# Optimization experiments

Hardware: AMD Instinct MI355X
Metric: run time of the kernel (lower is better)

The kernel has to match this reference:

```python
import jax, jax.numpy as jnp
import numpy as np

RHO = 1060.0   # blood density kg/m^3
DX = 1e-3      # grid spacing
CCFL = 0.9     # CFL number
EPS_A = 1e-6   # area floor


def setup_inputs() -> dict:
    key = jax.random.key(0)
    k0, k1, k2 = jax.random.split(key, 3)
    M = 90000          # 3 vessels x 30000 cells
    T = 150            # time steps
    Rs = jax.random.normal(k0, (4,), dtype=jnp.float32)
    sim_dat = jnp.ones((2, M), dtype=jnp.float32)            # row0: A, row1: Q seed
    sim_dat_const = jax.random.uniform(k1, (11, M), dtype=jnp.float32)
    input_data = jax.random.uniform(k2, (T,), dtype=jnp.float32)
    strides = jnp.array([[0, 30000], [30000, 60000], [60000, 90000]], dtype=jnp.int32)
    return {"Rs": Rs, "sim_dat": sim_dat, "sim_dat_const": sim_dat_const,
            "input_data": input_data, "strides": strides, "upper": T}


def reference(Rs, sim_dat, sim_dat_const, input_data, strides, upper):
    M = sim_dat.shape[1]
    # --- SimDense: softplus reparam of 4 resistance scale factors ---
    rs = jax.nn.softplus(Rs)
    idx = jnp.arange(M)
    m1 = (idx >= strides[1, 0]) & (idx < strides[1, 1])  # vessel 1 region
    m2 = (idx >= strides[2, 0]) & (idx < strides[2, 1])  # vessel 2 region
    # constant rows (shifted positive)
    A0 = sim_dat_const[0] + 0.5     # reference area
    beta = sim_dat_const[1] + 1.0   # wall stiffness
    R1 = sim_dat_const[7] + 0.5     # proximal resistance (VAR_INDEX_1)
    R2 = sim_dat_const[8] + 0.5     # distal resistance (VAR_INDEX_2)
    # scatter scaled resistances into vessel-1 / vessel-2 regions
    R1 = jnp.where(m1, rs[0] * R1, jnp.where(m2, rs[2] * R1, R1))
    R2 = jnp.where(m1, rs[1] * R2, jnp.where(m2, rs[3] * R2, R2))
    Rtot = R1 + R2

    A_init = sim_dat[0]
    Q_init = 0.1 * sim_dat[1]
    starts = strides[:, 0]
    ends = strides[:, 1] - 1
    mids = (strides[:, 0] + strides[:, 1]) // 2

    def step(carry, inflow):
        A, Q = carry
        A = jnp.maximum(A, EPS_A)
        sq = jnp.sqrt(A / A0)
        P = beta * (sq - 1.0)                 # tube-law pressure
        u = Q / A
        c = jnp.sqrt(0.5 * beta / RHO * sq)   # wave speed
        smax = jnp.max(jnp.abs(u) + c)
        dt = CCFL * DX / smax                 # CFL-limited timestep
        # conservative fluxes for (A, Q)
        F_A = Q
        F_Q = Q * u + beta / (3.0 * RHO * A0) * A * sq
        # Lax-Friedrichs interface fluxes
        fhA = 0.5 * (F_A[:-1] + F_A[1:]) - 0.5 * smax * (A[1:] - A[:-1])
        fhQ = 0.5 * (F_Q[:-1] + F_Q[1:]) - 0.5 * smax * (Q[1:] - Q[:-1])
        lam = dt / DX
        A_new = A.at[1:-1].add(-lam * (fhA[1:] - fhA[:-1]))
        Q_new = Q.at[1:-1].add(-lam * (fhQ[1:] - fhQ[:-1]))
        # inlet / junction BC: prescribed inflow at each vessel start
        Q_new = Q_new.at[starts].set(inflow)
        # outlet BC: resistive Windkessel Q = P / (R1 + R2)
        Q_new = Q_new.at[ends].set(P[ends] / Rtot[ends])
        A_new = jnp.maximum(A_new, EPS_A)
        return (A_new, Q_new), P[mids]          # record mid-vessel pressures

    _, p = jax.lax.scan(step, (A_init, Q_init), input_data)
    return p  # [upper, 3]
```

## Files before the change

kernel.cpp:

```cpp
#include <hip/hip_runtime.h>

static constexpr int MM  = 90000;
static constexpr int TT  = 150;
static constexpr int BS  = 256;
static constexpr int CPT = 4;
static constexpr int CPB = BS * CPT;
static constexpr int NB  = (MM + CPB - 1) / CPB;
static constexpr int WPB = BS / 64;
static constexpr int PAGE_U32 = 2048;
static constexpr int PAGE_U64 = 1024;

__device__ unsigned int       g_bmax_s[128][PAGE_U32];
__device__ unsigned long long g_edge_s[NB][PAGE_U64];
__device__ unsigned long long g_dummy64;

__device__ __forceinline__ float softplus_f(float x) {
    return fmaxf(x, 0.0f) + log1pf(expf(-fabsf(x)));
}
__device__ __forceinline__ unsigned long long packAQ(float A, float Q) {
    return ((unsigned long long)__float_as_uint(Q) << 32) | (unsigned long long)__float_as_uint(A);
}
#define AG_LOAD32(p)     __hip_atomic_load((p), __ATOMIC_RELAXED, __HIP_MEMORY_SCOPE_AGENT)
#define AG_LOAD64(p)     __hip_atomic_load((p), __ATOMIC_RELAXED, __HIP_MEMORY_SCOPE_AGENT)
#define AG_STORE32(p, v) __hip_atomic_store((p), (v), __ATOMIC_RELAXED, __HIP_MEMORY_SCOPE_AGENT)
#define AG_STORE64(p, v) __hip_atomic_store((p), (v), __ATOMIC_RELAXED, __HIP_MEMORY_SCOPE_AGENT)

__global__ void init_ws_kernel() {
    int i = blockIdx.x * blockDim.x + threadIdx.x;
    int stride = gridDim.x * blockDim.x;
    unsigned int* pb = &g_bmax_s[0][0];
    for (int j = i; j < 128 * PAGE_U32; j += stride)
        pb[j] = ((j / PAGE_U32) < NB) ? 0u : 1u;
    unsigned long long* pe = &g_edge_s[0][0];
    for (int j = i; j < NB * PAGE_U64; j += stride) pe[j] = 0ull;
    if (i == 0) g_dummy64 = ~0ull;
}

__global__ void __launch_bounds__(BS) sim_kernel(
    const float* __restrict__ Rs,
    const float* __restrict__ sim_dat,
    const float* __restrict__ sdc,
    const float* __restrict__ inflow,
    float* __restrict__ out)
{
    __shared__ float sE[2][WPB][2][3];
    __shared__ float sred[2][WPB];
    __shared__ float s_smaxv;
    __shared__ float s_hL[3], s_hR[3];
    __shared__ float s_inflow[TT];

    const int b    = blockIdx.x;
    const int tid  = threadIdx.x;
    const int wv   = tid >> 6;
    const int lane = tid & 63;
    const int base = b * CPB + tid * CPT;

    for (int j = tid; j < TT; j += BS) s_inflow[j] = inflow[j];

    float A[CPT], Q[CPT], A0v[CPT], bet[CPT], cbv[CPT], k2v[CPT], sq[CPT], FQ[CPT];
    bool  act[CPT];
    #pragma unroll
    for (int c = 0; c < CPT; ++c) {
        int i = base + c;
        act[c] = (i < MM);
        if (act[c]) {
            A[c]   = fmaxf(sim_dat[i], 1e-6f);
            Q[c]   = 0.1f * sim_dat[MM + i];
            A0v[c] = sdc[i] + 0.5f;
            bet[c] = sdc[MM + i] + 1.0f;
        } else { A[c] = 1.0f; Q[c] = 0.0f; A0v[c] = 1.0f; bet[c] = 1.0f; }
        cbv[c] = (0.5f * bet[c]) / 1060.0f;
        k2v[c] = bet[c] / (3180.0f * A0v[c]);
    }
    const bool isStart = (base == 0) | (base == 30000) | (base == 60000);
    const bool isEnd   = (base + 3 == 29999) | (base + 3 == 59999) | (base + 3 == 89999);
    const int midSlot = (base == 15000) ? 0 : (base == 45000) ? 1 : (base == 75000) ? 2 : -1;
    float Rtot = 1.0f;
    if (isEnd) {
        int i3 = base + 3;
        float R1 = sdc[7 * MM + i3] + 0.5f;
        float R2 = sdc[8 * MM + i3] + 0.5f;
        if (i3 == 59999)      { R1 *= softplus_f(Rs[0]); R2 *= softplus_f(Rs[1]); }
        else if (i3 == 89999) { R1 *= softplus_f(Rs[2]); R2 *= softplus_f(Rs[3]); }
        Rtot = R1 + R2;
    }

    const bool pubL = (tid == 0) && (b > 0);
    const bool pubR = (tid == BS - 1) && (b < NB - 1);
    const bool fixL = pubL;
    const bool fixR = pubR;

    float s4 = 0.0f;
    #pragma unroll
    for (int c = 0; c < CPT; ++c) {
        sq[c] = sqrtf(A[c] / A0v[c]);
        float u  = Q[c] / A[c];
        float cc = sqrtf(cbv[c] * sq[c]);
        FQ[c] = Q[c] * u + k2v[c] * A[c] * sq[c];
        s4 = fmaxf(s4, act[c] ? (fabsf(u) + cc) : 0.0f);
    }
    if (pubL) {
        AG_STORE64(&g_edge_s[b][0], packAQ(A[0], Q[0]));
        AG_STORE64(&g_edge_s[b][1], (unsigned long long)__float_as_uint(FQ[0]));
    }
    if (pubR) {
        AG_STORE64(&g_edge_s[b][2], packAQ(A[3], Q[3]));
        AG_STORE64(&g_edge_s[b][3], (unsigned long long)__float_as_uint(FQ[3]));
    }
    {
        float mm = s4;
        #pragma unroll
        for (int off = 32; off > 0; off >>= 1) mm = fmaxf(mm, __shfl_xor(mm, off, 64));
        if (lane == 0)       { sE[0][wv][0][0] = A[0]; sE[0][wv][0][1] = Q[0]; sE[0][wv][0][2] = FQ[0];
                               sred[0][wv] = mm; }
        else if (lane == 63) { sE[0][wv][1][0] = A[3]; sE[0][wv][1][1] = Q[3]; sE[0][wv][1][2] = FQ[3]; }
    }
    __syncthreads();
    if (wv == 0 && lane == 0) {
        float bm = fmaxf(fmaxf(sred[0][0], sred[0][1]), fmaxf(sred[0][2], sred[0][3]));
        AG_STORE32(&g_bmax_s[b][0], __float_as_uint(bm));
    }

    for (int t = 0; t < TT; ++t) {
        const int par = t & 1, npar = par ^ 1;

        float Am = __shfl_up(A[3], 1, 64),  Qm = __shfl_up(Q[3], 1, 64),  Fm = __shfl_up(FQ[3], 1, 64);
        float Ap = __shfl_down(A[0], 1, 64), Qp = __shfl_down(Q[0], 1, 64), Fp = __shfl_down(FQ[0], 1, 64);
        if (lane == 0 && wv > 0)       { Am = sE[par][wv-1][1][0]; Qm = sE[par][wv-1][1][1]; Fm = sE[par][wv-1][1][2]; }
        if (lane == 63 && wv < WPB - 1){ Ap = sE[par][wv+1][0][0]; Qp = sE[par][wv+1][0][1]; Fp = sE[par][wv+1][0][2]; }

        float dFA[CPT], lapA[CPT], dFQ[CPT], lapQ[CPT];
        #pragma unroll
        for (int c = 0; c < CPT; ++c) {
            float Al = (c == 0) ? Am : A[c-1],  Ql = (c == 0) ? Qm : Q[c-1],  Fl = (c == 0) ? Fm : FQ[c-1];
            float Ar = (c == 3) ? Ap : A[c+1],  Qr = (c == 3) ? Qp : Q[c+1],  Fr = (c == 3) ? Fp : FQ[c+1];
            dFA[c]  = 0.5f * (Qr - Ql);
            lapA[c] = 0.5f * (Ar - 2.0f * A[c] + Al);
            dFQ[c]  = 0.5f * (Fr - Fl);
            lapQ[c] = 0.5f * (Qr - 2.0f * Q[c] + Ql);
        }
        if (midSlot >= 0) out[t * 3 + midSlot] = bet[0] * (sq[0] - 1.0f);
        const float Pend = bet[3] * (sq[3] - 1.0f);

        if (wv == 0) {
            const unsigned long long* pE = &g_dummy64;
            const int t4 = t * 4;
            if (lane == 0 && b > 0)           pE = &g_edge_s[b - 1][t4 + 2];
            else if (lane == 1 && b > 0)      pE = &g_edge_s[b - 1][t4 + 3];
            else if (lane == 2 && b < NB - 1) pE = &g_edge_s[b + 1][t4 + 0];
            else if (lane == 3 && b < NB - 1) pE = &g_edge_s[b + 1][t4 + 1];
            unsigned int x0, x1;
            unsigned long long e64;
            for (;;) {
                x0  = AG_LOAD32(&g_bmax_s[lane][t]);
                x1  = AG_LOAD32(&g_bmax_s[64 + lane][t]);
                e64 = AG_LOAD64(pE);
                if (__all((x0 != 0u) & (x1 != 0u) & (e64 != 0ull))) break;
            }
            float ml = fmaxf(__uint_as_float(x0), __uint_as_float(x1));
            #pragma unroll
            for (int off = 32; off > 0; off >>= 1) ml = fmaxf(ml, __shfl_xor(ml, off, 64));
            if (lane == 0) s_smaxv = ml;
            if (lane == 0 && b > 0)           { s_hL[0] = __uint_as_float((unsigned int)e64);
                                                s_hL[1] = __uint_as_float((unsigned int)(e64 >> 32)); }
            else if (lane == 1 && b > 0)      { s_hL[2] = __uint_as_float((unsigned int)e64); }
            else if (lane == 2 && b < NB - 1) { s_hR[0] = __uint_as_float((unsigned int)e64);
                                                s_hR[1] = __uint_as_float((unsigned int)(e64 >> 32)); }
            else if (lane == 3 && b < NB - 1) { s_hR[2] = __uint_as_float((unsigned int)e64); }
        }
        __syncthreads();

        const float smax = s_smaxv;
        const float dt  = ((float)(0.9 * 0.001)) / smax;
        const float lam = dt / 0.001f;
        const float w   = lam * smax;

        if (fixL) {
            float Al = s_hL[0], Ql = s_hL[1], Fl = s_hL[2];
            dFA[0]  = 0.5f * (Q[1] - Ql);
            lapA[0] = 0.5f * (A[1] - 2.0f * A[0] + Al);
            dFQ[0]  = 0.5f * (FQ[1] - Fl);
            lapQ[0] = 0.5f * (Q[1] - 2.0f * Q[0] + Ql);
        }
        if (fixR) {
            float Ar = s_hR[0], Qr = s_hR[1], Fr = s_hR[2];
            dFA[3]  = 0.5f * (Qr - Q[2]);
            lapA[3] = 0.5f * (Ar - 2.0f * A[3] + A[2]);
            dFQ[3]  = 0.5f * (Fr - FQ[2]);
            lapQ[3] = 0.5f * (Qr - 2.0f * Q[3] + Q[2]);
        }
        #pragma unroll
        for (int c = 0; c < CPT; ++c) {
            int i = base + c;
            if (act[c] && i > 0 && i < MM - 1) {
                A[c] = fmaf(w, lapA[c], fmaf(-lam, dFA[c], A[c]));
                Q[c] = fmaf(w, lapQ[c], fmaf(-lam, dFQ[c], Q[c]));
            }
        }
        if (isStart) Q[0] = s_inflow[t];
        if (isEnd)   Q[3] = Pend / Rtot;
        #pragma unroll
        for (int c = 0; c < CPT; ++c) A[c] = fmaxf(A[c], 1e-6f);

        const int n4 = (t + 1) * 4;
        if (pubL) AG_STORE64(&g_edge_s[b][n4 + 0], packAQ(A[0], Q[0]));
        if (pubR) AG_STORE64(&g_edge_s[b][n4 + 2], packAQ(A[3], Q[3]));

        s4 = 0.0f;
        #pragma unroll
        for (int c = 0; c < CPT; ++c) {
            sq[c] = sqrtf(A[c] / A0v[c]);
            float u  = Q[c] / A[c];
            float cc = sqrtf(cbv[c] * sq[c]);
            FQ[c] = Q[c] * u + k2v[c] * A[c] * sq[c];
            s4 = fmaxf(s4, act[c] ? (fabsf(u) + cc) : 0.0f);
        }
        if (pubL) AG_STORE64(&g_edge_s[b][n4 + 1], (unsigned long long)__float_as_uint(FQ[0]));
        if (pubR) AG_STORE64(&g_edge_s[b][n4 + 3], (unsigned long long)__float_as_uint(FQ[3]));

        float mm = s4;
        #pragma unroll
        for (int off = 32; off > 0; off >>= 1) mm = fmaxf(mm, __shfl_xor(mm, off, 64));
        if (lane == 0)       { sE[npar][wv][0][0] = A[0]; sE[npar][wv][0][1] = Q[0]; sE[npar][wv][0][2] = FQ[0];
                               sred[npar][wv] = mm; }
        else if (lane == 63) { sE[npar][wv][1][0] = A[3]; sE[npar][wv][1][1] = Q[3]; sE[npar][wv][1][2] = FQ[3]; }
        __syncthreads();

        if (wv == 0 && lane == 0) {
            float bm = fmaxf(fmaxf(sred[npar][0], sred[npar][1]), fmaxf(sred[npar][2], sred[npar][3]));
            AG_STORE32(&g_bmax_s[b][t + 1], __float_as_uint(bm));
        }
    }
}

extern "C" void kernel_launch(void* const* d_in, const int* in_sizes, int n_in,
                              void* d_out, int out_size, void* d_ws, size_t ws_size,
                              hipStream_t stream) {
    (void)in_sizes; (void)n_in; (void)d_ws; (void)ws_size; (void)out_size;

    const float* Rs      = (const float*)d_in[0];
    const float* sim_dat = (const float*)d_in[1];
    const float* sdc     = (const float*)d_in[2];
    const float* inflow  = (const float*)d_in[3];
    float* out = (float*)d_out;

    hipLaunchKernelGGL(init_ws_kernel, dim3(240), dim3(256), 0, stream);

    hipLaunchKernelGGL(sim_kernel, dim3(NB), dim3(BS), 0, stream,
                       Rs, sim_dat, sdc, inflow, out);
}
```

Measured before the change: 478.3 us.

## Publish per-wave max directly and drop second per-step block barrier

Each wave now writes its own max wave speed to a global slot (a wider table of 352 wave entries), so the block no longer needs a second __syncthreads to combine wave maxima before publishing. The wave reductions use DPP row operations instead of shuffles. Global polling loads are issued before the stencil work so their latency overlaps computation. Intra-block halo fixups are deferred to after the single barrier. The wave max is published before FQ is computed, which gets the signal out earlier. The cost is six loads per lane per poll instead of two, and more traffic on the global max table.

```diff
diff --git a/kernel.cpp b/kernel.cpp
--- a/kernel.cpp
+++ b/kernel.cpp
@@ -7,10 +7,12 @@
 static constexpr int CPB = BS * CPT;
 static constexpr int NB  = (MM + CPB - 1) / CPB;
 static constexpr int WPB = BS / 64;
+static constexpr int NWAVE  = NB * WPB;
+static constexpr int WPAGES = 384;
 static constexpr int PAGE_U32 = 2048;
 static constexpr int PAGE_U64 = 1024;
 
-__device__ unsigned int       g_bmax_s[128][PAGE_U32];
+__device__ unsigned int       g_wmax[WPAGES][PAGE_U32];
 __device__ unsigned long long g_edge_s[NB][PAGE_U64];
 __device__ unsigned long long g_dummy64;
 
@@ -25,12 +27,25 @@
 #define AG_STORE32(p, v) __hip_atomic_store((p), (v), __ATOMIC_RELAXED, __HIP_MEMORY_SCOPE_AGENT)
 #define AG_STORE64(p, v) __hip_atomic_store((p), (v), __ATOMIC_RELAXED, __HIP_MEMORY_SCOPE_AGENT)
 
+#define DPP_MAX(x, ctrl, rm, bm)                                                     \
+    x = fmaxf(x, __int_as_float(__builtin_amdgcn_update_dpp(                          \
+                     0, __float_as_int(x), (ctrl), (rm), (bm), true)))
+__device__ __forceinline__ float wave_max64(float x) {
+    DPP_MAX(x, 0x111, 0xf, 0xf);
+    DPP_MAX(x, 0x112, 0xf, 0xf);
+    DPP_MAX(x, 0x114, 0xf, 0xe);
+    DPP_MAX(x, 0x118, 0xf, 0xc);
+    DPP_MAX(x, 0x142, 0xa, 0xf);
+    DPP_MAX(x, 0x143, 0xc, 0xf);
+    return x;
+}
+
 __global__ void init_ws_kernel() {
     int i = blockIdx.x * blockDim.x + threadIdx.x;
     int stride = gridDim.x * blockDim.x;
-    unsigned int* pb = &g_bmax_s[0][0];
-    for (int j = i; j < 128 * PAGE_U32; j += stride)
-        pb[j] = ((j / PAGE_U32) < NB) ? 0u : 1u;
+    unsigned int* pw = &g_wmax[0][0];
+    for (int j = i; j < WPAGES * PAGE_U32; j += stride)
+        pw[j] = ((j / PAGE_U32) < NWAVE) ? 0u : 1u;
     unsigned long long* pe = &g_edge_s[0][0];
     for (int j = i; j < NB * PAGE_U64; j += stride) pe[j] = 0ull;
     if (i == 0) g_dummy64 = ~0ull;
@@ -44,8 +59,7 @@
     float* __restrict__ out)
 {
     __shared__ float sE[2][WPB][2][3];
-    __shared__ float sred[2][WPB];
-    __shared__ float s_smaxv;
+    __shared__ float s_bc[2];
     __shared__ float s_hL[3], s_hR[3];
     __shared__ float s_inflow[TT];
 
@@ -54,6 +68,7 @@
     const int wv   = tid >> 6;
     const int lane = tid & 63;
     const int base = b * CPB + tid * CPT;
+    const int gw   = b * WPB + wv;
 
     for (int j = tid; j < TT; j += BS) s_inflow[j] = inflow[j];
 
@@ -87,17 +102,17 @@
 
     const bool pubL = (tid == 0) && (b > 0);
     const bool pubR = (tid == BS - 1) && (b < NB - 1);
-    const bool fixL = pubL;
-    const bool fixR = pubR;
+
+    const unsigned int* pwl = &g_wmax[lane][0];
 
     float s4 = 0.0f;
     #pragma unroll
     for (int c = 0; c < CPT; ++c) {
         sq[c] = sqrtf(A[c] / A0v[c]);
-        float u  = Q[c] / A[c];
+        float uu = Q[c] / A[c];
         float cc = sqrtf(cbv[c] * sq[c]);
-        FQ[c] = Q[c] * u + k2v[c] * A[c] * sq[c];
-        s4 = fmaxf(s4, act[c] ? (fabsf(u) + cc) : 0.0f);
+        FQ[c] = Q[c] * uu + k2v[c] * A[c] * sq[c];
+        s4 = fmaxf(s4, act[c] ? (fabsf(uu) + cc) : 0.0f);
     }
     if (pubL) {
         AG_STORE64(&g_edge_s[b][0], packAQ(A[0], Q[0]));
@@ -108,26 +123,36 @@
         AG_STORE64(&g_edge_s[b][3], (unsigned long long)__float_as_uint(FQ[3]));
     }
     {
-        float mm = s4;
-        #pragma unroll
-        for (int off = 32; off > 0; off >>= 1) mm = fmaxf(mm, __shfl_xor(mm, off, 64));
-        if (lane == 0)       { sE[0][wv][0][0] = A[0]; sE[0][wv][0][1] = Q[0]; sE[0][wv][0][2] = FQ[0];
-                               sred[0][wv] = mm; }
-        else if (lane == 63) { sE[0][wv][1][0] = A[3]; sE[0][wv][1][1] = Q[3]; sE[0][wv][1][2] = FQ[3]; }
-    }
-    __syncthreads();
-    if (wv == 0 && lane == 0) {
-        float bm = fmaxf(fmaxf(sred[0][0], sred[0][1]), fmaxf(sred[0][2], sred[0][3]));
-        AG_STORE32(&g_bmax_s[b][0], __float_as_uint(bm));
-    }
+        float red = wave_max64(s4);
+        if (lane == 63) AG_STORE32(&g_wmax[gw][0], __float_as_uint(red));
+    }
+    if (lane == 0)       { sE[0][wv][0][0] = A[0]; sE[0][wv][0][1] = Q[0]; sE[0][wv][0][2] = FQ[0]; }
+    else if (lane == 63) { sE[0][wv][1][0] = A[3]; sE[0][wv][1][1] = Q[3]; sE[0][wv][1][2] = FQ[3]; }
 
     for (int t = 0; t < TT; ++t) {
         const int par = t & 1, npar = par ^ 1;
 
+        unsigned int x0, x1, x2, x3, x4, x5;
+        unsigned long long e64;
+        const unsigned long long* pE = &g_dummy64;
+        if (wv == 0) {
+            const int t4 = t * 4;
+            if (lane == 0 && b > 0)           pE = &g_edge_s[b - 1][t4 + 2];
+            else if (lane == 1 && b > 0)      pE = &g_edge_s[b - 1][t4 + 3];
+            else if (lane == 2 && b < NB - 1) pE = &g_edge_s[b + 1][t4 + 0];
+            else if (lane == 3 && b < NB - 1) pE = &g_edge_s[b + 1][t4 + 1];
+            const unsigned int* p = pwl + t;
+            x0 = AG_LOAD32(p);
+            x1 = AG_LOAD32(p +  64 * PAGE_U32);
+            x2 = AG_LOAD32(p + 128 * PAGE_U32);
+            x3 = AG_LOAD32(p + 192 * PAGE_U32);
+            x4 = AG_LOAD32(p + 256 * PAGE_U32);
+            x5 = AG_LOAD32(p + 320 * PAGE_U32);
+            e64 = AG_LOAD64(pE);
+        }
+
         float Am = __shfl_up(A[3], 1, 64),  Qm = __shfl_up(Q[3], 1, 64),  Fm = __shfl_up(FQ[3], 1, 64);
         float Ap = __shfl_down(A[0], 1, 64), Qp = __shfl_down(Q[0], 1, 64), Fp = __shfl_down(FQ[0], 1, 64);
-        if (lane == 0 && wv > 0)       { Am = sE[par][wv-1][1][0]; Qm = sE[par][wv-1][1][1]; Fm = sE[par][wv-1][1][2]; }
-        if (lane == 63 && wv < WPB - 1){ Ap = sE[par][wv+1][0][0]; Qp = sE[par][wv+1][0][1]; Fp = sE[par][wv+1][0][2]; }
 
         float dFA[CPT], lapA[CPT], dFQ[CPT], lapQ[CPT];
         #pragma unroll
@@ -140,55 +165,64 @@
             lapQ[c] = 0.5f * (Qr - 2.0f * Q[c] + Ql);
         }
         if (midSlot >= 0) out[t * 3 + midSlot] = bet[0] * (sq[0] - 1.0f);
-        const float Pend = bet[3] * (sq[3] - 1.0f);
+        float qFix = 0.0f;
+        if (isStart) qFix = s_inflow[t];
+        if (isEnd)   qFix = (bet[3] * (sq[3] - 1.0f)) / Rtot;
 
         if (wv == 0) {
-            const unsigned long long* pE = &g_dummy64;
-            const int t4 = t * 4;
-            if (lane == 0 && b > 0)           pE = &g_edge_s[b - 1][t4 + 2];
-            else if (lane == 1 && b > 0)      pE = &g_edge_s[b - 1][t4 + 3];
-            else if (lane == 2 && b < NB - 1) pE = &g_edge_s[b + 1][t4 + 0];
-            else if (lane == 3 && b < NB - 1) pE = &g_edge_s[b + 1][t4 + 1];
-            unsigned int x0, x1;
-            unsigned long long e64;
-            for (;;) {
-                x0  = AG_LOAD32(&g_bmax_s[lane][t]);
-                x1  = AG_LOAD32(&g_bmax_s[64 + lane][t]);
+            const unsigned int* p = pwl + t;
+            bool ok = __all((x0 != 0u) & (x1 != 0u) & (x2 != 0u) & (x3 != 0u) &
+                            (x4 != 0u) & (x5 != 0u) & (e64 != 0ull));
+            while (!ok) {
+                x0 = AG_LOAD32(p);
+                x1 = AG_LOAD32(p +  64 * PAGE_U32);
+                x2 = AG_LOAD32(p + 128 * PAGE_U32);
+                x3 = AG_LOAD32(p + 192 * PAGE_U32);
+                x4 = AG_LOAD32(p + 256 * PAGE_U32);
+                x5 = AG_LOAD32(p + 320 * PAGE_U32);
                 e64 = AG_LOAD64(pE);
-                if (__all((x0 != 0u) & (x1 != 0u) & (e64 != 0ull))) break;
+                ok = __all((x0 != 0u) & (x1 != 0u) & (x2 != 0u) & (x3 != 0u) &
+                           (x4 != 0u) & (x5 != 0u) & (e64 != 0ull));
             }
-            float ml = fmaxf(__uint_as_float(x0), __uint_as_float(x1));
-            #pragma unroll
-            for (int off = 32; off > 0; off >>= 1) ml = fmaxf(ml, __shfl_xor(ml, off, 64));
-            if (lane == 0) s_smaxv = ml;
             if (lane == 0 && b > 0)           { s_hL[0] = __uint_as_float((unsigned int)e64);
                                                 s_hL[1] = __uint_as_float((unsigned int)(e64 >> 32)); }
             else if (lane == 1 && b > 0)      { s_hL[2] = __uint_as_float((unsigned int)e64); }
             else if (lane == 2 && b < NB - 1) { s_hR[0] = __uint_as_float((unsigned int)e64);
                                                 s_hR[1] = __uint_as_float((unsigned int)(e64 >> 32)); }
             else if (lane == 3 && b < NB - 1) { s_hR[2] = __uint_as_float((unsigned int)e64); }
+            float m = fmaxf(fmaxf(fmaxf(__uint_as_float(x0), __uint_as_float(x1)),
+                                  fmaxf(__uint_as_float(x2), __uint_as_float(x3))),
+                            fmaxf(__uint_as_float(x4), __uint_as_float(x5)));
+            m = wave_max64(m);
+            const float smax = __int_as_float(__builtin_amdgcn_readlane(__float_as_int(m), 63));
+            const float dt  = ((float)(0.9 * 0.001)) / smax;
+            const float lam = dt / 0.001f;
+            const float w   = lam * smax;
+            if (lane == 0) { s_bc[0] = lam; s_bc[1] = w; }
         }
         __syncthreads();
-
-        const float smax = s_smaxv;
-        const float dt  = ((float)(0.9 * 0.001)) / smax;
-        const float lam = dt / 0.001f;
-        const float w   = lam * smax;
-
-        if (fixL) {
-            float Al = s_hL[0], Ql = s_hL[1], Fl = s_hL[2];
+        const float lam = s_bc[0];
+        const float w   = s_bc[1];
+
+        if (lane == 0 && (wv > 0 || b > 0)) {
+            float Al, Ql, Fl;
+            if (wv > 0) { Al = sE[par][wv-1][1][0]; Ql = sE[par][wv-1][1][1]; Fl = sE[par][wv-1][1][2]; }
+            else        { Al = s_hL[0];             Ql = s_hL[1];             Fl = s_hL[2]; }
             dFA[0]  = 0.5f * (Q[1] - Ql);
             lapA[0] = 0.5f * (A[1] - 2.0f * A[0] + Al);
             dFQ[0]  = 0.5f * (FQ[1] - Fl);
             lapQ[0] = 0.5f * (Q[1] - 2.0f * Q[0] + Ql);
         }
-        if (fixR) {
-            float Ar = s_hR[0], Qr = s_hR[1], Fr = s_hR[2];
+        if (lane == 63 && (wv < WPB - 1 || b < NB - 1)) {
+            float Ar, Qr, Fr;
+            if (wv < WPB - 1) { Ar = sE[par][wv+1][0][0]; Qr = sE[par][wv+1][0][1]; Fr = sE[par][wv+1][0][2]; }
+            else              { Ar = s_hR[0];             Qr = s_hR[1];             Fr = s_hR[2]; }
             dFA[3]  = 0.5f * (Qr - Q[2]);
             lapA[3] = 0.5f * (Ar - 2.0f * A[3] + A[2]);
             dFQ[3]  = 0.5f * (Fr - FQ[2]);
             lapQ[3] = 0.5f * (Qr - 2.0f * Q[3] + Q[2]);
         }
+
         #pragma unroll
         for (int c = 0; c < CPT; ++c) {
             int i = base + c;
@@ -197,8 +231,8 @@
                 Q[c] = fmaf(w, lapQ[c], fmaf(-lam, dFQ[c], Q[c]));
             }
         }
-        if (isStart) Q[0] = s_inflow[t];
-        if (isEnd)   Q[3] = Pend / Rtot;
+        if (isStart) Q[0] = qFix;
+        if (isEnd)   Q[3] = qFix;
         #pragma unroll
         for (int c = 0; c < CPT; ++c) A[c] = fmaxf(A[c], 1e-6f);
 
@@ -206,30 +240,28 @@
         if (pubL) AG_STORE64(&g_edge_s[b][n4 + 0], packAQ(A[0], Q[0]));
         if (pubR) AG_STORE64(&g_edge_s[b][n4 + 2], packAQ(A[3], Q[3]));
 
+        float uu[CPT];
         s4 = 0.0f;
         #pragma unroll
         for (int c = 0; c < CPT; ++c) {
             sq[c] = sqrtf(A[c] / A0v[c]);
-            float u  = Q[c] / A[c];
+            uu[c] = Q[c] / A[c];
             float cc = sqrtf(cbv[c] * sq[c]);
-            FQ[c] = Q[c] * u + k2v[c] * A[c] * sq[c];
-            s4 = fmaxf(s4, act[c] ? (fabsf(u) + cc) : 0.0f);
-        }
+            s4 = fmaxf(s4, act[c] ? (fabsf(uu[c]) + cc) : 0.0f);
+        }
+        {
+            float red = wave_max64(s4);
+            if (lane == 63) AG_STORE32(&g_wmax[gw][t + 1], __float_as_uint(red));
+        }
+        #pragma unroll
+        for (int c = 0; c < CPT; ++c)
+            FQ[c] = Q[c] * uu[c] + k2v[c] * A[c] * sq[c];
+
         if (pubL) AG_STORE64(&g_edge_s[b][n4 + 1], (unsigned long long)__float_as_uint(FQ[0]));
         if (pubR) AG_STORE64(&g_edge_s[b][n4 + 3], (unsigned long long)__float_as_uint(FQ[3]));
 
-        float mm = s4;
-        #pragma unroll
-        for (int off = 32; off > 0; off >>= 1) mm = fmaxf(mm, __shfl_xor(mm, off, 64));
-        if (lane == 0)       { sE[npar][wv][0][0] = A[0]; sE[npar][wv][0][1] = Q[0]; sE[npar][wv][0][2] = FQ[0];
-                               sred[npar][wv] = mm; }
+        if (lane == 0)       { sE[npar][wv][0][0] = A[0]; sE[npar][wv][0][1] = Q[0]; sE[npar][wv][0][2] = FQ[0]; }
         else if (lane == 63) { sE[npar][wv][1][0] = A[3]; sE[npar][wv][1][1] = Q[3]; sE[npar][wv][1][2] = FQ[3]; }
-        __syncthreads();
-
-        if (wv == 0 && lane == 0) {
-            float bm = fmaxf(fmaxf(sred[npar][0], sred[npar][1]), fmaxf(sred[npar][2], sred[npar][3]));
-            AG_STORE32(&g_bmax_s[b][t + 1], __float_as_uint(bm));
-        }
     }
 }
 
```

Result: faster. 459.9 us (-3.8%).
